# Optimization experiments

Hardware: AMD Instinct MI355X
Metric: run time of the kernel (lower is better)

## Reference

```python
import jax, jax.numpy as jnp
import numpy as np

T, B, D, H, F, E = 2048, 2, 1024, 16, 4096, 8
HD = D // H
EPS = 1.1920929e-07  # torch.finfo(float32).eps


def setup_inputs() -> dict:
    key = jax.random.key(0)
    ks = jax.random.split(key, 20)
    sc = D ** -0.5
    n = lambda k, shape, s: jax.random.normal(k, shape, jnp.float32) * s
    return {
        "x": jax.random.normal(ks[0], (T, B, D), jnp.float32),
        "Wq": n(ks[1], (D, D), sc), "bq": jnp.zeros((D,), jnp.float32),
        "Wk": n(ks[2], (D, D), sc), "bk": jnp.zeros((D,), jnp.float32),
        "Wv": n(ks[3], (D, D), sc), "bv": jnp.zeros((D,), jnp.float32),
        "Wo": n(ks[4], (D, D), sc), "bo": jnp.zeros((D,), jnp.float32),
        "ln1_g": jnp.ones((D,), jnp.float32), "ln1_b": jnp.zeros((D,), jnp.float32),
        "ln2_g": jnp.ones((D,), jnp.float32), "ln2_b": jnp.zeros((D,), jnp.float32),
        "wg": n(ks[5], (D, E), sc),
        "W1": n(ks[6], (E, D, F), sc), "b1": jnp.zeros((E, F), jnp.float32),
        "W2": n(ks[7], (E, F, D), F ** -0.5), "b2": jnp.zeros((E, D), jnp.float32),
    }


def layer_norm(x, g, b):
    m = jnp.mean(x, -1, keepdims=True)
    v = jnp.var(x, -1, keepdims=True)
    return (x - m) * jax.lax.rsqrt(v + 1e-5) * g + b


def attention(x, Wq, bq, Wk, bk, Wv, bv, Wo, bo):
    t, b, d = x.shape
    q = ((x @ Wq + bq) * (HD ** -0.5)).reshape(t, b, H, HD)
    k = (x @ Wk + bk).reshape(t, b, H, HD)
    v = (x @ Wv + bv).reshape(t, b, H, HD)
    a = jax.nn.softmax(jnp.einsum('tbhd,sbhd->bhts', q, k), axis=-1)
    o = jnp.einsum('bhts,sbhd->tbhd', a, v).reshape(t, b, d)
    return o @ Wo + bo


def moe(xf, wg, W1, b1, W2, b2):
    # xf: [S, D] tokens (batch-major order, matching x.transpose(0,1).reshape(-1,d))
    S = xf.shape[0]
    C = 2 * ((S + E - 1) // E)  # fairseq top2 train capacity
    logits = xf.astype(jnp.float32) @ wg.astype(jnp.float32)
    gates = jax.nn.softmax(logits, axis=-1)
    idx1 = jnp.argmax(gates, axis=-1)
    m1 = jax.nn.one_hot(idx1, E, dtype=jnp.int32)
    idx2 = jnp.argmax(jnp.where(m1 > 0, -jnp.inf, logits), axis=-1)
    m2 = jax.nn.one_hot(idx2, E, dtype=jnp.int32)
    g1 = jnp.take_along_axis(gates, idx1[:, None], 1)[:, 0]
    g2 = jnp.take_along_axis(gates, idx2[:, None], 1)[:, 0]
    loc1 = jnp.cumsum(m1, axis=0) - 1
    loc2 = jnp.cumsum(m2, axis=0) - 1 + jnp.sum(m1, axis=0, keepdims=True)
    pos1 = jnp.sum(loc1 * m1, axis=1)
    pos2 = jnp.sum(loc2 * m2, axis=1)
    l_aux = jnp.mean(jnp.mean(gates, 0) * jnp.mean(m1.astype(jnp.float32), 0)) * E * E
    k1 = (pos1 < C).astype(xf.dtype)
    k2 = (pos2 < C).astype(xf.dtype)
    g1 = g1.astype(xf.dtype) * k1
    g2 = g2.astype(xf.dtype) * k2
    den = jnp.maximum(g1 + g2, EPS)
    g1, g2 = g1 / den, g2 / den
    f1 = idx1 * C + jnp.minimum(pos1, C - 1)
    f2 = idx2 * C + jnp.minimum(pos2, C - 1)
    # dispatch (unweighted, capacity-masked)
    buf = jnp.zeros((E * C, D), xf.dtype)
    buf = buf.at[f1].add(xf * k1[:, None]).at[f2].add(xf * k2[:, None])
    h = jax.nn.relu(jnp.einsum('ecd,edf->ecf', buf.reshape(E, C, D), W1) + b1[:, None, :])
    out = (jnp.einsum('ecf,efd->ecd', h, W2) + b2[:, None, :]).reshape(E * C, D)
    # combine with normalized gates (dropped tokens have zero gate)
    y = g1[:, None] * out[f1] + g2[:, None] * out[f2]
    return y, l_aux


def reference(x, Wq, bq, Wk, bk, Wv, bv, Wo, bo, ln1_g, ln1_b, ln2_g, ln2_b, wg, W1, b1, W2, b2):
    # pre-LN self-attention block
    residual = x
    h = layer_norm(x, ln1_g, ln1_b)
    h = attention(h, Wq, bq, Wk, bk, Wv, bv, Wo, bo)
    x = residual + h
    # pre-LN MoE FFN block
    residual = x
    h = layer_norm(x, ln2_g, ln2_b)
    hb = jnp.swapaxes(h, 0, 1).reshape(-1, D)  # [B*T, D]
    y, l_aux = moe(hb, wg, W1, b1, W2, b2)
    y = jnp.swapaxes(y.reshape(B, T, D), 0, 1)
    x = residual + y
    return x, l_aux
```

## Files before the change

### kernel.cpp

```cpp
#include <hip/hip_runtime.h>

#define TT 2048
#define BB 2
#define DD 1024
#define HH 16
#define HD 64
#define FF 4096
#define EE 8
#define SS (TT*BB)
#define CAP 1024
#define EPSF 1.1920929e-07f

typedef __attribute__((ext_vector_type(8))) short short8;
typedef __attribute__((ext_vector_type(4))) float floatx4;

static __device__ inline unsigned short f2bf(float f){
    unsigned int u = __float_as_uint(f);
    unsigned int r = (u + 0x7fffu + ((u>>16)&1u)) >> 16;
    return (unsigned short)r;
}
static __device__ inline float bf2f(unsigned short h){
    return __uint_as_float(((unsigned int)h)<<16);
}
static __device__ inline void split2(float x, unsigned short& h, unsigned short& l){
    unsigned short hh = f2bf(x);
    h = hh;
    l = f2bf(x - bf2f(hh));
}
#define GETF4(v,j) ((j)==0?(v).x:(j)==1?(v).y:(j)==2?(v).z:(v).w)

__global__ __launch_bounds__(256) void ln_kernel(const float* __restrict__ x,
    const float* __restrict__ gam, const float* __restrict__ bet, float* __restrict__ o)
{
    int row = blockIdx.x;
    int tid = threadIdx.x;
    float4 v = ((const float4*)(x + (size_t)row*DD))[tid];
    float s  = v.x+v.y+v.z+v.w;
    float ss = v.x*v.x+v.y*v.y+v.z*v.z+v.w*v.w;
    __shared__ float r1[256], r2[256];
    r1[tid]=s; r2[tid]=ss;
    __syncthreads();
    for (int off=128; off>0; off>>=1){
        if (tid<off){ r1[tid]+=r1[tid+off]; r2[tid]+=r2[tid+off]; }
        __syncthreads();
    }
    float mean = r1[0] * (1.f/DD);
    float var  = r2[0] * (1.f/DD) - mean*mean;
    float inv  = 1.f / sqrtf(var + 1e-5f);
    float4 g = ((const float4*)gam)[tid];
    float4 b = ((const float4*)bet)[tid];
    float4 r;
    r.x = (v.x-mean)*inv*g.x + b.x;
    r.y = (v.y-mean)*inv*g.y + b.y;
    r.z = (v.z-mean)*inv*g.z + b.z;
    r.w = (v.w-mean)*inv*g.w + b.w;
    ((float4*)(o + (size_t)row*DD))[tid] = r;
}

template<bool RELU, bool OUTBF16>
__global__ __launch_bounds__(256) void gemm_mfma(
    const unsigned short* __restrict__ A, const unsigned short* __restrict__ Bt,
    const float* __restrict__ bias, float* __restrict__ Cf,
    unsigned short* __restrict__ Cb,
    int M, int N, int K, long wStride, int bStride, int rowsPerExp)
{
    __shared__ unsigned short As[128*64];
    __shared__ unsigned short Bs[128*64];
    const int tid = threadIdx.x, lane = tid&63;
    const int w = tid>>6, wr = w>>1, wc = w&1;
    const int m0 = blockIdx.y*128, n0 = blockIdx.x*128;
    const int e = m0 / rowsPerExp;
    const unsigned short* Bp = Bt + (size_t)e*wStride;
    const int srow = tid>>3, sslot = tid&7;
    floatx4 zf = {0.f,0.f,0.f,0.f};
    floatx4 acc[4][4];
    #pragma unroll
    for (int m=0;m<4;m++)
        #pragma unroll
        for (int n=0;n<4;n++) acc[m][n]=zf;

    short8 ar[4], br[4];
    #pragma unroll
    for (int i=0;i<4;i++){
        int r = srow + i*32;
        ar[i] = *(const short8*)(A  + (size_t)(m0+r)*K + sslot*8);
        br[i] = *(const short8*)(Bp + (size_t)(n0+r)*K + sslot*8);
    }
    const int NT = K/64;
    for (int kt=0; kt<NT; kt++){
        __syncthreads();
        #pragma unroll
        for (int i=0;i<4;i++){
            int r = srow + i*32;
            int off = r*64 + ((sslot ^ (r&7))<<3);
            *(short8*)(&As[off]) = ar[i];
            *(short8*)(&Bs[off]) = br[i];
        }
        __syncthreads();
        if (kt+1 < NT){
            int k0 = (kt+1)*64;
            #pragma unroll
            for (int i=0;i<4;i++){
                int r = srow + i*32;
                ar[i] = *(const short8*)(A  + (size_t)(m0+r)*K + k0 + sslot*8);
                br[i] = *(const short8*)(Bp + (size_t)(n0+r)*K + k0 + sslot*8);
            }
        }
        #pragma unroll
        for (int kk=0;kk<2;kk++){
            short8 af[4], bf[4];
            int kgrp = kk*4 + (lane>>4);
            #pragma unroll
            for (int m=0;m<4;m++){
                int rowa = wr*64 + m*16 + (lane&15);
                af[m] = *(const short8*)(&As[rowa*64 + ((kgrp ^ (rowa&7))<<3)]);
                int rowb = wc*64 + m*16 + (lane&15);
                bf[m] = *(const short8*)(&Bs[rowb*64 + ((kgrp ^ (rowb&7))<<3)]);
            }
            #pragma unroll
            for (int m=0;m<4;m++)
                #pragma unroll
                for (int n=0;n<4;n++)
                    acc[m][n] = __builtin_amdgcn_mfma_f32_16x16x32_bf16(af[m], bf[n], acc[m][n], 0,0,0);
        }
    }
    int colg = n0 + wc*64 + (lane&15);
    int rowg = m0 + wr*64 + ((lane>>4)<<2);
    #pragma unroll
    for (int n=0;n<4;n++){
        float bv = bias[e*bStride + colg + n*16];
        #pragma unroll
        for (int m=0;m<4;m++){
            #pragma unroll
            for (int i2=0;i2<4;i2++){
                float v = acc[m][n][i2] + bv;
                if (RELU) v = fmaxf(v, 0.f);
                size_t o = (size_t)(rowg + m*16 + i2)*N + colg + n*16;
                if (OUTBF16) Cb[o] = f2bf(v); else Cf[o] = v;
            }
        }
    }
}

template<bool QKV>
__global__ __launch_bounds__(256) void gemm_mfma_s(
    const float* __restrict__ A,
    const unsigned short* __restrict__ Bhi, const unsigned short* __restrict__ Blo,
    const float* __restrict__ b0, const float* __restrict__ b1p, const float* __restrict__ b2p,
    const float* __restrict__ res,
    float* __restrict__ o0, float* __restrict__ o1, float* __restrict__ o2,
    int M, int K)
{
    __shared__ unsigned short As[128*64];
    __shared__ unsigned short Bs[128*64];
    const int tid = threadIdx.x, lane = tid&63;
    const int w = tid>>6, wr = w>>1, wc = w&1;
    const int m0 = blockIdx.y*128, n0 = blockIdx.x*128;
    const int row = tid>>1, khalf = tid&1;
    floatx4 zf = {0.f,0.f,0.f,0.f};
    floatx4 acc[4][4];
    #pragma unroll
    for (int m=0;m<4;m++)
        #pragma unroll
        for (int n=0;n<4;n++) acc[m][n]=zf;

    float4 aw0,aw1,aw2,aw3;
    short8 bwh0,bwh1,bwl0,bwl1;
    {
        const float* ap = A + (size_t)(m0+row)*K + khalf*16;
        aw0 = ((const float4*)ap)[0]; aw1 = ((const float4*)ap)[1];
        aw2 = ((const float4*)ap)[2]; aw3 = ((const float4*)ap)[3];
        const unsigned short* bh = Bhi + (size_t)(n0+row)*K + khalf*16;
        const unsigned short* bl = Blo + (size_t)(n0+row)*K + khalf*16;
        bwh0 = *(const short8*)(bh); bwh1 = *(const short8*)(bh+8);
        bwl0 = *(const short8*)(bl); bwl1 = *(const short8*)(bl+8);
    }
    const int NT = K/32;
    for (int kt=0; kt<NT; kt++){
        __syncthreads();
        {
            unsigned short h[16], l[16];
            #pragma unroll
            for (int j=0;j<4;j++){ split2(GETF4(aw0,j), h[j],   l[j]); }
            #pragma unroll
            for (int j=0;j<4;j++){ split2(GETF4(aw1,j), h[4+j], l[4+j]); }
            #pragma unroll
            for (int j=0;j<4;j++){ split2(GETF4(aw2,j), h[8+j], l[8+j]); }
            #pragma unroll
            for (int j=0;j<4;j++){ split2(GETF4(aw3,j), h[12+j],l[12+j]); }
            int base = row*64, sw = row&7;
            int g0 = khalf*2, g1 = khalf*2+1;
            *(short8*)(&As[base + ((g0^sw)<<3)])     = *(short8*)(&h[0]);
            *(short8*)(&As[base + ((g1^sw)<<3)])     = *(short8*)(&h[8]);
            *(short8*)(&As[base + (((g0+4)^sw)<<3)]) = *(short8*)(&l[0]);
            *(short8*)(&As[base + (((g1+4)^sw)<<3)]) = *(short8*)(&l[8]);
            *(short8*)(&Bs[base + ((g0^sw)<<3)])     = bwh0;
            *(short8*)(&Bs[base + ((g1^sw)<<3)])     = bwh1;
            *(short8*)(&Bs[base + (((g0+4)^sw)<<3)]) = bwl0;
            *(short8*)(&Bs[base + (((g1+4)^sw)<<3)]) = bwl1;
        }
        __syncthreads();
        if (kt+1 < NT){
            int k0 = (kt+1)*32;
            const float* ap = A + (size_t)(m0+row)*K + k0 + khalf*16;
            aw0 = ((const float4*)ap)[0]; aw1 = ((const float4*)ap)[1];
            aw2 = ((const float4*)ap)[2]; aw3 = ((const float4*)ap)[3];
            const unsigned short* bh = Bhi + (size_t)(n0+row)*K + k0 + khalf*16;
            const unsigned short* bl = Blo + (size_t)(n0+row)*K + k0 + khalf*16;
            bwh0 = *(const short8*)(bh); bwh1 = *(const short8*)(bh+8);
            bwl0 = *(const short8*)(bl); bwl1 = *(const short8*)(bl+8);
        }
        {
            int kg = lane>>4;
            short8 afh[4], afl[4], bfh[4], bfl[4];
            #pragma unroll
            for (int m=0;m<4;m++){
                int ra = wr*64 + m*16 + (lane&15);
                afh[m] = *(const short8*)(&As[ra*64 + ((kg ^ (ra&7))<<3)]);
                afl[m] = *(const short8*)(&As[ra*64 + (((kg+4) ^ (ra&7))<<3)]);
                int rb = wc*64 + m*16 + (lane&15);
                bfh[m] = *(const short8*)(&Bs[rb*64 + ((kg ^ (rb&7))<<3)]);
                bfl[m] = *(const short8*)(&Bs[rb*64 + (((kg+4) ^ (rb&7))<<3)]);
            }
            #pragma unroll
            for (int m=0;m<4;m++)
                #pragma unroll
                for (int n=0;n<4;n++){
                    acc[m][n] = __builtin_amdgcn_mfma_f32_16x16x32_bf16(afl[m], bfl[n], acc[m][n], 0,0,0);
                    acc[m][n] = __builtin_amdgcn_mfma_f32_16x16x32_bf16(afl[m], bfh[n], acc[m][n], 0,0,0);
                    acc[m][n] = __builtin_amdgcn_mfma_f32_16x16x32_bf16(afh[m], bfl[n], acc[m][n], 0,0,0);
                    acc[m][n] = __builtin_amdgcn_mfma_f32_16x16x32_bf16(afh[m], bfh[n], acc[m][n], 0,0,0);
                }
        }
    }
    int colg = n0 + wc*64 + (lane&15);
    int rowg = m0 + wr*64 + ((lane>>4)<<2);
    const float* bp; float* op; float scale; int colc;
    if (QKV){
        int chunk = n0>>10;
        bp = chunk==0 ? b0 : (chunk==1 ? b1p : b2p);
        op = chunk==0 ? o0 : (chunk==1 ? o1 : o2);
        scale = chunk==0 ? 0.125f : 1.0f;
        colc = colg & 1023;
    } else { bp = b0; op = o0; scale = 1.0f; colc = colg; }
    #pragma unroll
    for (int n=0;n<4;n++){
        float bv = bp[colc + n*16];
        #pragma unroll
        for (int m=0;m<4;m++){
            #pragma unroll
            for (int i2=0;i2<4;i2++){
                float v = (acc[m][n][i2] + bv)*scale;
                int r = rowg + m*16 + i2;
                if (!QKV) v += res[(size_t)r*DD + colc + n*16];
                op[(size_t)r*DD + colc + n*16] = v;
            }
        }
    }
}

__global__ __launch_bounds__(256) void attn_mfma(const float* __restrict__ q,
    const float* __restrict__ k, const float* __restrict__ v, float* __restrict__ o)
{
    __shared__ unsigned short Kh[64*64], Kl[64*64];
    __shared__ unsigned short Vh[64*64], Vl[64*64];
    __shared__ unsigned short Ph[4*16*64], Pl[4*16*64];
    const int tid = threadIdx.x, lane = tid&63, w = tid>>6;
    const int t0 = blockIdx.x*64;
    const int b = blockIdx.y>>4, h = blockIdx.y&15;

    short8 qh[2], ql[2];
    #pragma unroll
    for (int kk=0;kk<2;kk++){
        const float* qp = q + ((size_t)(t0 + 16*w + (lane&15))*BB + b)*DD + h*64 + kk*32 + (lane>>4)*8;
        float4 f0 = ((const float4*)qp)[0];
        float4 f1 = ((const float4*)qp)[1];
        unsigned short hh[8], ll[8];
        #pragma unroll
        for (int j=0;j<4;j++){ split2(GETF4(f0,j), hh[j], ll[j]); }
        #pragma unroll
        for (int j=0;j<4;j++){ split2(GETF4(f1,j), hh[4+j], ll[4+j]); }
        qh[kk] = *(short8*)hh; ql[kk] = *(short8*)ll;
    }

    const int kr = tid>>2, kq = tid&3;
    const int vs0 = (tid&15)*4, vd0 = (tid>>4)*4;
    float4 kw0,kw1,kw2,kw3, vw0,vw1,vw2,vw3;
    {
        const float* kp = k + ((size_t)(0 + kr)*BB + b)*DD + h*64 + kq*16;
        kw0=((const float4*)kp)[0]; kw1=((const float4*)kp)[1];
        kw2=((const float4*)kp)[2]; kw3=((const float4*)kp)[3];
        const float* vp = v + ((size_t)(0 + vs0)*BB + b)*DD + h*64 + vd0;
        vw0=*(const float4*)(vp);
        vw1=*(const float4*)(vp + (size_t)BB*DD);
        vw2=*(const float4*)(vp + (size_t)2*BB*DD);
        vw3=*(const float4*)(vp + (size_t)3*BB*DD);
    }

    float m_st[4] = {-3.0e38f,-3.0e38f,-3.0e38f,-3.0e38f};
    float l_st[4] = {0.f,0.f,0.f,0.f};
    floatx4 zf = {0.f,0.f,0.f,0.f};
    floatx4 oacc[4]; 
    #pragma unroll
    for (int n=0;n<4;n++) oacc[n]=zf;

    for (int s0=0; s0<TT; s0+=64){
        __syncthreads();
        {
            unsigned short hh[16], ll[16];
            #pragma unroll
            for (int j=0;j<4;j++){ split2(GETF4(kw0,j), hh[j],   ll[j]); }
            #pragma unroll
            for (int j=0;j<4;j++){ split2(GETF4(kw1,j), hh[4+j], ll[4+j]); }
            #pragma unroll
            for (int j=0;j<4;j++){ split2(GETF4(kw2,j), hh[8+j], ll[8+j]); }
            #pragma unroll
            for (int j=0;j<4;j++){ split2(GETF4(kw3,j), hh[12+j],ll[12+j]); }
            int base = kr*64, sw = kr&7;
            int g0 = kq*2, g1 = kq*2+1;
            *(short8*)(&Kh[base + ((g0^sw)<<3)]) = *(short8*)(&hh[0]);
            *(short8*)(&Kh[base + ((g1^sw)<<3)]) = *(short8*)(&hh[8]);
            *(short8*)(&Kl[base + ((g0^sw)<<3)]) = *(short8*)(&ll[0]);
            *(short8*)(&Kl[base + ((g1^sw)<<3)]) = *(short8*)(&ll[8]);
        }
        {
            int g = vs0>>3, so = vs0&7;
            #pragma unroll
            for (int j=0;j<4;j++){
                int d = vd0 + j;
                unsigned short h0,h1,h2,h3, l0,l1,l2,l3;
                split2(GETF4(vw0,j), h0,l0);
                split2(GETF4(vw1,j), h1,l1);
                split2(GETF4(vw2,j), h2,l2);
                split2(GETF4(vw3,j), h3,l3);
                ushort4 hv; hv.x=h0; hv.y=h1; hv.z=h2; hv.w=h3;
                ushort4 lv; lv.x=l0; lv.y=l1; lv.z=l2; lv.w=l3;
                int off = d*64 + ((g ^ (d&7))<<3) + so;
                *(ushort4*)(&Vh[off]) = hv;
                *(ushort4*)(&Vl[off]) = lv;
            }
        }
        __syncthreads();
        if (s0+64 < TT){
            const float* kp = k + ((size_t)(s0+64 + kr)*BB + b)*DD + h*64 + kq*16;
            kw0=((const float4*)kp)[0]; kw1=((const float4*)kp)[1];
            kw2=((const float4*)kp)[2]; kw3=((const float4*)kp)[3];
            const float* vp = v + ((size_t)(s0+64 + vs0)*BB + b)*DD + h*64 + vd0;
            vw0=*(const float4*)(vp);
            vw1=*(const float4*)(vp + (size_t)BB*DD);
            vw2=*(const float4*)(vp + (size_t)2*BB*DD);
            vw3=*(const float4*)(vp + (size_t)3*BB*DD);
        }
        floatx4 sacc[4];
        #pragma unroll
        for (int n=0;n<4;n++){
            floatx4 s = zf;
            #pragma unroll
            for (int kk=0;kk<2;kk++){
                int g = kk*4 + (lane>>4);
                int rb = n*16 + (lane&15);
                short8 kbh = *(const short8*)(&Kh[rb*64 + ((g ^ (rb&7))<<3)]);
                short8 kbl = *(const short8*)(&Kl[rb*64 + ((g ^ (rb&7))<<3)]);
                s = __builtin_amdgcn_mfma_f32_16x16x32_bf16(ql[kk], kbl, s, 0,0,0);
                s = __builtin_amdgcn_mfma_f32_16x16x32_bf16(ql[kk], kbh, s, 0,0,0);
                s = __builtin_amdgcn_mfma_f32_16x16x32_bf16(qh[kk], kbl, s, 0,0,0);
                s = __builtin_amdgcn_mfma_f32_16x16x32_bf16(qh[kk], kbh, s, 0,0,0);
            }
            sacc[n] = s;
        }
        float mx[4];
        #pragma unroll
        for (int r=0;r<4;r++)
            mx[r] = fmaxf(fmaxf(sacc[0][r], sacc[1][r]), fmaxf(sacc[2][r], sacc[3][r]));
        #pragma unroll
        for (int sh=1; sh<16; sh<<=1){
            #pragma unroll
            for (int r=0;r<4;r++) mx[r] = fmaxf(mx[r], __shfl_xor(mx[r], sh));
        }
        float corr[4];
        #pragma unroll
        for (int r=0;r<4;r++){
            float nm = fmaxf(m_st[r], mx[r]);
            corr[r] = __expf(m_st[r] - nm);
            m_st[r] = nm;
        }
        float ts[4] = {0.f,0.f,0.f,0.f};
        #pragma unroll
        for (int n=0;n<4;n++){
            #pragma unroll
            for (int r=0;r<4;r++){
                float p = __expf(sacc[n][r] - m_st[r]);
                ts[r] += p;
                unsigned short ph, pl;
                split2(p, ph, pl);
                int q2 = ((lane>>4)<<2) + r;
                int s2 = n*16 + (lane&15);
                int off = w*1024 + q2*64 + (((s2>>3) ^ (q2&7))<<3) + (s2&7);
                Ph[off] = ph; Pl[off] = pl;
            }
        }
        #pragma unroll
        for (int sh=1; sh<16; sh<<=1){
            #pragma unroll
            for (int r=0;r<4;r++) ts[r] += __shfl_xor(ts[r], sh);
        }
        #pragma unroll
        for (int r=0;r<4;r++) l_st[r] = l_st[r]*corr[r] + ts[r];
        #pragma unroll
        for (int n=0;n<4;n++)
            #pragma unroll
            for (int r=0;r<4;r++) oacc[n][r] *= corr[r];
        #pragma unroll
        for (int kk=0;kk<2;kk++){
            int g = kk*4 + (lane>>4);
            int rq = lane&15;
            short8 pah = *(const short8*)(&Ph[w*1024 + rq*64 + ((g ^ (rq&7))<<3)]);
            short8 pal = *(const short8*)(&Pl[w*1024 + rq*64 + ((g ^ (rq&7))<<3)]);
            #pragma unroll
            for (int n=0;n<4;n++){
                int rd = n*16 + (lane&15);
                short8 vbh = *(const short8*)(&Vh[rd*64 + ((g ^ (rd&7))<<3)]);
                short8 vbl = *(const short8*)(&Vl[rd*64 + ((g ^ (rd&7))<<3)]);
                oacc[n] = __builtin_amdgcn_mfma_f32_16x16x32_bf16(pal, vbl, oacc[n], 0,0,0);
                oacc[n] = __builtin_amdgcn_mfma_f32_16x16x32_bf16(pal, vbh, oacc[n], 0,0,0);
                oacc[n] = __builtin_amdgcn_mfma_f32_16x16x32_bf16(pah, vbl, oacc[n], 0,0,0);
                oacc[n] = __builtin_amdgcn_mfma_f32_16x16x32_bf16(pah, vbh, oacc[n], 0,0,0);
            }
        }
    }
    float il[4];
    #pragma unroll
    for (int r=0;r<4;r++) il[r] = 1.f/l_st[r];
    int qrow = t0 + 16*w + ((lane>>4)<<2);
    #pragma unroll
    for (int n=0;n<4;n++){
        #pragma unroll
        for (int r=0;r<4;r++){
            o[((size_t)(qrow+r)*BB + b)*DD + h*64 + n*16 + (lane&15)] = oacc[n][r]*il[r];
        }
    }
}

__global__ __launch_bounds__(256) void transpose_bf16_k(const float* __restrict__ in,
    unsigned short* __restrict__ outp, int R, int C)
{
    __shared__ float t[64][65];
    int e = blockIdx.z;
    const float* ip = in + (size_t)e*R*C;
    unsigned short* op = outp + (size_t)e*R*C;
    int r0 = blockIdx.y*64, c0 = blockIdx.x*64;
    int tid = threadIdx.x;
    #pragma unroll
    for (int i=0;i<4;i++){
        int ch = i*256 + tid;
        int r = ch>>4, c4 = (ch&15)*4;
        float4 v = *(const float4*)(ip + (size_t)(r0+r)*C + c0 + c4);
        t[r][c4+0]=v.x; t[r][c4+1]=v.y; t[r][c4+2]=v.z; t[r][c4+3]=v.w;
    }
    __syncthreads();
    #pragma unroll
    for (int i=0;i<4;i++){
        int ch = i*256 + tid;
        int rr = ch>>4, c4 = (ch&15)*4;
        ushort4 o;
        o.x = f2bf(t[c4+0][rr]); o.y = f2bf(t[c4+1][rr]);
        o.z = f2bf(t[c4+2][rr]); o.w = f2bf(t[c4+3][rr]);
        *(ushort4*)(op + (size_t)(c0+rr)*R + r0 + c4) = o;
    }
}

__global__ __launch_bounds__(256) void transpose_split_k(const float* __restrict__ in,
    unsigned short* __restrict__ oh, unsigned short* __restrict__ ol, int R, int C)
{
    __shared__ float t[64][65];
    int r0 = blockIdx.y*64, c0 = blockIdx.x*64;
    int tid = threadIdx.x;
    #pragma unroll
    for (int i=0;i<4;i++){
        int ch = i*256 + tid;
        int r = ch>>4, c4 = (ch&15)*4;
        float4 v = *(const float4*)(in + (size_t)(r0+r)*C + c0 + c4);
        t[r][c4+0]=v.x; t[r][c4+1]=v.y; t[r][c4+2]=v.z; t[r][c4+3]=v.w;
    }
    __syncthreads();
    #pragma unroll
    for (int i=0;i<4;i++){
        int ch = i*256 + tid;
        int rr = ch>>4, c4 = (ch&15)*4;
        ushort4 hv, lv;
        split2(t[c4+0][rr], hv.x, lv.x);
        split2(t[c4+1][rr], hv.y, lv.y);
        split2(t[c4+2][rr], hv.z, lv.z);
        split2(t[c4+3][rr], hv.w, lv.w);
        size_t off = (size_t)(c0+rr)*R + r0 + c4;
        *(ushort4*)(oh + off) = hv;
        *(ushort4*)(ol + off) = lv;
    }
}

__global__ __launch_bounds__(256) void gather_bf16_k(const float* __restrict__ h2,
    const int* __restrict__ s2r, unsigned short* __restrict__ buf)
{
    int s = blockIdx.x; int row = s2r[s]; int c = threadIdx.x;
    float4 v = make_float4(0.f,0.f,0.f,0.f);
    if (row>=0) v = *(const float4*)(h2 + (size_t)row*DD + c*4);
    ushort4 o;
    o.x=f2bf(v.x); o.y=f2bf(v.y); o.z=f2bf(v.z); o.w=f2bf(v.w);
    *(ushort4*)(buf + (size_t)s*DD + c*4) = o;
}

__global__ __launch_bounds__(256) void route_kernel(const float* __restrict__ h2,
    const float* __restrict__ wgm, float* __restrict__ gates,
    int* __restrict__ idx1, int* __restrict__ idx2,
    float* __restrict__ g1, float* __restrict__ g2)
{
    int wid = threadIdx.x >> 6, lane = threadIdx.x & 63;
    int s = blockIdx.x*4 + wid;
    int row = (s % TT)*BB + (s / TT);
    const float* hr = h2 + (size_t)row*DD;
    float acc[EE] = {};
    #pragma unroll
    for (int c=0;c<16;c++){
        int d = c*64 + lane;
        float xv = hr[d];
        const float* wr = wgm + (size_t)d*EE;
        #pragma unroll
        for (int e2=0;e2<EE;e2++) acc[e2] += xv * wr[e2];
    }
    #pragma unroll
    for (int off=32; off>0; off>>=1){
        #pragma unroll
        for (int e2=0;e2<EE;e2++) acc[e2] += __shfl_down(acc[e2], off);
    }
    if (lane==0){
        float mx = acc[0];
        #pragma unroll
        for (int e2=1;e2<EE;e2++) mx = fmaxf(mx, acc[e2]);
        float ex[EE]; float sum=0.f;
        #pragma unroll
        for (int e2=0;e2<EE;e2++){ ex[e2] = __expf(acc[e2]-mx); sum += ex[e2]; }
        float inv = 1.f/sum;
        int i1=0; float bv1=acc[0];
        #pragma unroll
        for (int e2=1;e2<EE;e2++){ if (acc[e2] > bv1){ bv1=acc[e2]; i1=e2; } }
        int i2=-1; float bv2=-3.0e38f;
        #pragma unroll
        for (int e2=0;e2<EE;e2++){ if (e2!=i1 && acc[e2] > bv2){ bv2=acc[e2]; i2=e2; } }
        #pragma unroll
        for (int e2=0;e2<EE;e2++) gates[(size_t)s*EE + e2] = ex[e2]*inv;
        idx1[s]=i1; idx2[s]=i2;
        g1[s]=ex[i1]*inv; g2[s]=ex[i2]*inv;
    }
}

__global__ __launch_bounds__(256) void scan_kernel(
    const float* __restrict__ gates, const int* __restrict__ idx1, const int* __restrict__ idx2,
    const float* __restrict__ g1, const float* __restrict__ g2,
    float* __restrict__ g1n, float* __restrict__ g2n,
    int* __restrict__ f1, int* __restrict__ f2, int* __restrict__ slot2row,
    float* __restrict__ laux)
{
    __shared__ int i1s[SS];
    __shared__ int i2s[SS];
    __shared__ int cnt1[256][EE];
    __shared__ int cnt2[256][EE];
    __shared__ float gsum[256][EE];
    __shared__ int tot1[EE];
    int tid = threadIdx.x;
    for (int i=tid;i<EE*CAP;i+=256) slot2row[i] = -1;
    for (int i=tid;i<SS;i+=256){ i1s[i]=idx1[i]; i2s[i]=idx2[i]; }
    __syncthreads();
    int c1l[EE]={}, c2l[EE]={};
    float gl[EE]={};
    int base = tid*16;
    for (int qq=0;qq<16;qq++){
        int s = base+qq;
        c1l[i1s[s]]++; c2l[i2s[s]]++;
        #pragma unroll
        for (int e2=0;e2<EE;e2++) gl[e2] += gates[(size_t)s*EE+e2];
    }
    #pragma unroll
    for (int e2=0;e2<EE;e2++){ cnt1[tid][e2]=c1l[e2]; cnt2[tid][e2]=c2l[e2]; gsum[tid][e2]=gl[e2]; }
    __syncthreads();
    if (tid < EE){
        int e2 = tid;
        int run=0;
        for (int t=0;t<256;t++){ int tmp=cnt1[t][e2]; cnt1[t][e2]=run; run+=tmp; }
        tot1[e2]=run;
        run=0;
        for (int t=0;t<256;t++){ int tmp=cnt2[t][e2]; cnt2[t][e2]=run; run+=tmp; }
        float gr=0.f;
        for (int t=0;t<256;t++) gr += gsum[t][e2];
        gsum[0][e2]=gr;
    }
    __syncthreads();
    int p1[EE], p2[EE];
    #pragma unroll
    for (int e2=0;e2<EE;e2++){ p1[e2]=cnt1[tid][e2]; p2[e2]=cnt2[tid][e2]+tot1[e2]; }
    for (int qq=0;qq<16;qq++){
        int s = base+qq;
        int e1 = i1s[s], e2v = i2s[s];
        int pos1 = p1[e1]++;
        int pos2 = p2[e2v]++;
        float gv1 = g1[s], gv2 = g2[s];
        float gm1 = (pos1<CAP)? gv1 : 0.f;
        float gm2 = (pos2<CAP)? gv2 : 0.f;
        float den = fmaxf(gm1+gm2, EPSF);
        g1n[s] = gm1/den; g2n[s] = gm2/den;
        int ff1 = e1*CAP + (pos1<CAP?pos1:CAP-1);
        int ff2 = e2v*CAP + (pos2<CAP?pos2:CAP-1);
        f1[s]=ff1; f2[s]=ff2;
        int hrow = (s % TT)*BB + (s / TT);
        if (pos1<CAP) slot2row[ff1]=hrow;
        if (pos2<CAP) slot2row[ff2]=hrow;
    }
    if (tid==0){
        float a=0.f;
        #pragma unroll
        for (int e2=0;e2<EE;e2++) a += (gsum[0][e2]*(1.f/SS)) * ((float)tot1[e2]*(1.f/SS));
        laux[0] = a * (float)EE;
    }
}

__global__ __launch_bounds__(256) void combine_kernel(const float* __restrict__ x2,
    const float* __restrict__ eout, const float* __restrict__ g1n, const float* __restrict__ g2n,
    const int* __restrict__ f1, const int* __restrict__ f2, float* __restrict__ out)
{
    int s = blockIdx.x;
    float a = g1n[s], b = g2n[s];
    int s1 = f1[s], s2 = f2[s];
    int row = (s % TT)*BB + (s / TT);
    int c = threadIdx.x;
    float4 o1 = ((const float4*)(eout + (size_t)s1*DD))[c];
    float4 o2 = ((const float4*)(eout + (size_t)s2*DD))[c];
    float4 xr = ((const float4*)(x2 + (size_t)row*DD))[c];
    float4 r;
    r.x = xr.x + a*o1.x + b*o2.x;
    r.y = xr.y + a*o1.y + b*o2.y;
    r.z = xr.z + a*o1.z + b*o2.z;
    r.w = xr.w + a*o1.w + b*o2.w;
    ((float4*)(out + (size_t)row*DD))[c] = r;
}

extern "C" void kernel_launch(void* const* d_in, const int* in_sizes, int n_in,
                              void* d_out, int out_size, void* d_ws, size_t ws_size,
                              hipStream_t stream)
{
    const float* x    = (const float*)d_in[0];
    const float* Wq   = (const float*)d_in[1];
    const float* bq   = (const float*)d_in[2];
    const float* Wk   = (const float*)d_in[3];
    const float* bk   = (const float*)d_in[4];
    const float* Wv   = (const float*)d_in[5];
    const float* bv   = (const float*)d_in[6];
    const float* Wo   = (const float*)d_in[7];
    const float* bo   = (const float*)d_in[8];
    const float* ln1g = (const float*)d_in[9];
    const float* ln1b = (const float*)d_in[10];
    const float* ln2g = (const float*)d_in[11];
    const float* ln2b = (const float*)d_in[12];
    const float* wgm  = (const float*)d_in[13];
    const float* W1   = (const float*)d_in[14];
    const float* b1   = (const float*)d_in[15];
    const float* W2   = (const float*)d_in[16];
    const float* b2   = (const float*)d_in[17];
    float* out = (float*)d_out;

    char* w = (char*)d_ws;
    float*          h1   = (float*)(w);
    float*          qb   = (float*)(w + ((size_t)16<<20));
    float*          kb   = (float*)(w + ((size_t)32<<20));
    float*          vb   = (float*)(w + ((size_t)48<<20));
    float*          x2   = (float*)(w + ((size_t)64<<20));
    unsigned short* bufb = (unsigned short*)(w + ((size_t)80<<20));
    unsigned short* hb   = (unsigned short*)(w + ((size_t)96<<20));
    unsigned short* Bqkv_hi = (unsigned short*)(w + ((size_t)96<<20));
    unsigned short* Bqkv_lo = (unsigned short*)(w + ((size_t)102<<20));
    unsigned short* Bo_hi   = (unsigned short*)(w + ((size_t)108<<20));
    unsigned short* Bo_lo   = (unsigned short*)(w + ((size_t)110<<20));
    unsigned short* W1t  = (unsigned short*)(w + ((size_t)160<<20));
    unsigned short* W2t  = (unsigned short*)(w + ((size_t)224<<20));
    float*          ffno = kb;
    char*  sm   = w + ((size_t)288<<20);
    float* gates   = (float*)(sm);                sm += (size_t)SS*EE*4;
    int*   idx1    = (int*)(sm);                  sm += SS*4;
    int*   idx2    = (int*)(sm);                  sm += SS*4;
    float* g1      = (float*)(sm);                sm += SS*4;
    float* g2      = (float*)(sm);                sm += SS*4;
    float* g1n     = (float*)(sm);                sm += SS*4;
    float* g2n     = (float*)(sm);                sm += SS*4;
    int*   f1      = (int*)(sm);                  sm += SS*4;
    int*   f2      = (int*)(sm);                  sm += SS*4;
    int*   slot2row= (int*)(sm);                  sm += EE*CAP*4;

    transpose_bf16_k<<<dim3(FF/64, DD/64, EE), 256, 0, stream>>>(W1, W1t, DD, FF);
    transpose_bf16_k<<<dim3(DD/64, FF/64, EE), 256, 0, stream>>>(W2, W2t, FF, DD);
    transpose_split_k<<<dim3(16,16), 256, 0, stream>>>(Wq, Bqkv_hi,                Bqkv_lo,                DD, DD);
    transpose_split_k<<<dim3(16,16), 256, 0, stream>>>(Wk, Bqkv_hi + (size_t)DD*DD,   Bqkv_lo + (size_t)DD*DD,   DD, DD);
    transpose_split_k<<<dim3(16,16), 256, 0, stream>>>(Wv, Bqkv_hi + (size_t)2*DD*DD, Bqkv_lo + (size_t)2*DD*DD, DD, DD);
    transpose_split_k<<<dim3(16,16), 256, 0, stream>>>(Wo, Bo_hi, Bo_lo, DD, DD);
    ln_kernel<<<SS, 256, 0, stream>>>(x, ln1g, ln1b, h1);
    gemm_mfma_s<true><<<dim3(24, SS/128), 256, 0, stream>>>(
        h1, Bqkv_hi, Bqkv_lo, bq, bk, bv, nullptr, qb, kb, vb, SS, DD);
    attn_mfma<<<dim3(TT/64, BB*HH), 256, 0, stream>>>(qb, kb, vb, h1);
    gemm_mfma_s<false><<<dim3(8, SS/128), 256, 0, stream>>>(
        h1, Bo_hi, Bo_lo, bo, bo, bo, x, x2, x2, x2, SS, DD);
    ln_kernel<<<SS, 256, 0, stream>>>(x2, ln2g, ln2b, qb);
    route_kernel<<<SS/4, 256, 0, stream>>>(qb, wgm, gates, idx1, idx2, g1, g2);
    scan_kernel<<<1, 256, 0, stream>>>(gates, idx1, idx2, g1, g2,
        g1n, g2n, f1, f2, slot2row, out + (size_t)SS*DD);
    gather_bf16_k<<<EE*CAP, 256, 0, stream>>>(qb, slot2row, bufb);
    gemm_mfma<true,true><<<dim3(FF/128, (EE*CAP)/128), 256, 0, stream>>>(
        bufb, W1t, b1, nullptr, hb, EE*CAP, FF, DD, (long)FF*DD, FF, CAP);
    gemm_mfma<false,false><<<dim3(DD/128, (EE*CAP)/128), 256, 0, stream>>>(
        hb, W2t, b2, ffno, nullptr, EE*CAP, DD, FF, (long)DD*FF, DD, CAP);
    combine_kernel<<<SS, 256, 0, stream>>>(x2, ffno, g1n, g2n, f1, f2, out);
    (void)in_sizes; (void)n_in; (void)out_size; (void)ws_size;
}
```

Before: 686.7 us.

## Drop lo*lo MFMA terms and pre-split K/V into bf16 hi/lo in QKV epilogue

Removes the low-times-low MFMA term from the split-bf16 GEMMs and from the attention QK and PV products, cutting matrix work by a quarter. The QKV GEMM epilogue now writes K and V directly as bf16 hi/lo pairs, so attention loads half-width data and skips its per-tile split. Truncation-based splitting replaces round-to-nearest for activations and P, which makes the splits cheaper. The trade is slightly lower precision and more work in the QKV epilogue.

Measured after the change: 681.5 us. Within noise of the previous version (-0.8%).

```diff
diff --git a/kernel.cpp b/kernel.cpp
--- a/kernel.cpp
+++ b/kernel.cpp
@@ -27,7 +27,15 @@
     h = hh;
     l = f2bf(x - bf2f(hh));
 }
+static __device__ inline void split2t(float x, unsigned short& h, unsigned short& l){
+    unsigned int u = __float_as_uint(x);
+    unsigned int hu = u & 0xffff0000u;
+    h = (unsigned short)(hu>>16);
+    float r = x - __uint_as_float(hu);
+    l = (unsigned short)(__float_as_uint(r)>>16);
+}
 #define GETF4(v,j) ((j)==0?(v).x:(j)==1?(v).y:(j)==2?(v).z:(v).w)
+#define GETU4(v,j) ((j)==0?(v).x:(j)==1?(v).y:(j)==2?(v).z:(v).w)
 
 __global__ __launch_bounds__(256) void ln_kernel(const float* __restrict__ x,
     const float* __restrict__ gam, const float* __restrict__ bet, float* __restrict__ o)
@@ -148,7 +156,9 @@
     const unsigned short* __restrict__ Bhi, const unsigned short* __restrict__ Blo,
     const float* __restrict__ b0, const float* __restrict__ b1p, const float* __restrict__ b2p,
     const float* __restrict__ res,
-    float* __restrict__ o0, float* __restrict__ o1, float* __restrict__ o2,
+    float* __restrict__ o0,
+    unsigned short* __restrict__ kh, unsigned short* __restrict__ kl,
+    unsigned short* __restrict__ vh, unsigned short* __restrict__ vl,
     int M, int K)
 {
     __shared__ unsigned short As[128*64];
@@ -181,13 +191,13 @@
         {
             unsigned short h[16], l[16];
             #pragma unroll
-            for (int j=0;j<4;j++){ split2(GETF4(aw0,j), h[j],   l[j]); }
-            #pragma unroll
-            for (int j=0;j<4;j++){ split2(GETF4(aw1,j), h[4+j], l[4+j]); }
-            #pragma unroll
-            for (int j=0;j<4;j++){ split2(GETF4(aw2,j), h[8+j], l[8+j]); }
-            #pragma unroll
-            for (int j=0;j<4;j++){ split2(GETF4(aw3,j), h[12+j],l[12+j]); }
+            for (int j=0;j<4;j++){ split2t(GETF4(aw0,j), h[j],   l[j]); }
+            #pragma unroll
+            for (int j=0;j<4;j++){ split2t(GETF4(aw1,j), h[4+j], l[4+j]); }
+            #pragma unroll
+            for (int j=0;j<4;j++){ split2t(GETF4(aw2,j), h[8+j], l[8+j]); }
+            #pragma unroll
+            for (int j=0;j<4;j++){ split2t(GETF4(aw3,j), h[12+j],l[12+j]); }
             int base = row*64, sw = row&7;
             int g0 = khalf*2, g1 = khalf*2+1;
             *(short8*)(&As[base + ((g0^sw)<<3)])     = *(short8*)(&h[0]);
@@ -226,7 +236,6 @@
             for (int m=0;m<4;m++)
                 #pragma unroll
                 for (int n=0;n<4;n++){
-                    acc[m][n] = __builtin_amdgcn_mfma_f32_16x16x32_bf16(afl[m], bfl[n], acc[m][n], 0,0,0);
                     acc[m][n] = __builtin_amdgcn_mfma_f32_16x16x32_bf16(afl[m], bfh[n], acc[m][n], 0,0,0);
                     acc[m][n] = __builtin_amdgcn_mfma_f32_16x16x32_bf16(afh[m], bfl[n], acc[m][n], 0,0,0);
                     acc[m][n] = __builtin_amdgcn_mfma_f32_16x16x32_bf16(afh[m], bfh[n], acc[m][n], 0,0,0);
@@ -235,32 +244,52 @@
     }
     int colg = n0 + wc*64 + (lane&15);
     int rowg = m0 + wr*64 + ((lane>>4)<<2);
-    const float* bp; float* op; float scale; int colc;
     if (QKV){
         int chunk = n0>>10;
-        bp = chunk==0 ? b0 : (chunk==1 ? b1p : b2p);
-        op = chunk==0 ? o0 : (chunk==1 ? o1 : o2);
-        scale = chunk==0 ? 0.125f : 1.0f;
-        colc = colg & 1023;
-    } else { bp = b0; op = o0; scale = 1.0f; colc = colg; }
-    #pragma unroll
-    for (int n=0;n<4;n++){
-        float bv = bp[colc + n*16];
-        #pragma unroll
-        for (int m=0;m<4;m++){
-            #pragma unroll
-            for (int i2=0;i2<4;i2++){
-                float v = (acc[m][n][i2] + bv)*scale;
-                int r = rowg + m*16 + i2;
-                if (!QKV) v += res[(size_t)r*DD + colc + n*16];
-                op[(size_t)r*DD + colc + n*16] = v;
+        int colc = colg & 1023;
+        const float* bp = chunk==0 ? b0 : (chunk==1 ? b1p : b2p);
+        #pragma unroll
+        for (int n=0;n<4;n++){
+            float bv = bp[colc + n*16];
+            #pragma unroll
+            for (int m=0;m<4;m++){
+                #pragma unroll
+                for (int i2=0;i2<4;i2++){
+                    int r = rowg + m*16 + i2;
+                    float v = acc[m][n][i2] + bv;
+                    size_t off = (size_t)r*DD + colc + n*16;
+                    if (chunk==0){
+                        o0[off] = v*0.125f;
+                    } else {
+                        unsigned short hh, ll;
+                        split2(v, hh, ll);
+                        if (chunk==1){ kh[off]=hh; kl[off]=ll; }
+                        else         { vh[off]=hh; vl[off]=ll; }
+                    }
+                }
+            }
+        }
+    } else {
+        #pragma unroll
+        for (int n=0;n<4;n++){
+            float bv = b0[colg + n*16];
+            #pragma unroll
+            for (int m=0;m<4;m++){
+                #pragma unroll
+                for (int i2=0;i2<4;i2++){
+                    int r = rowg + m*16 + i2;
+                    float v = acc[m][n][i2] + bv + res[(size_t)r*DD + colg + n*16];
+                    o0[(size_t)r*DD + colg + n*16] = v;
+                }
             }
         }
     }
 }
 
 __global__ __launch_bounds__(256) void attn_mfma(const float* __restrict__ q,
-    const float* __restrict__ k, const float* __restrict__ v, float* __restrict__ o)
+    const unsigned short* __restrict__ khi, const unsigned short* __restrict__ klo,
+    const unsigned short* __restrict__ vhi, const unsigned short* __restrict__ vlo,
+    float* __restrict__ o)
 {
     __shared__ unsigned short Kh[64*64], Kl[64*64];
     __shared__ unsigned short Vh[64*64], Vl[64*64];
@@ -285,56 +314,46 @@
 
     const int kr = tid>>2, kq = tid&3;
     const int vs0 = (tid&15)*4, vd0 = (tid>>4)*4;
-    float4 kw0,kw1,kw2,kw3, vw0,vw1,vw2,vw3;
+    short8 kwh0,kwh1,kwl0,kwl1;
+    ushort4 vwh[4], vwl[4];
     {
-        const float* kp = k + ((size_t)(0 + kr)*BB + b)*DD + h*64 + kq*16;
-        kw0=((const float4*)kp)[0]; kw1=((const float4*)kp)[1];
-        kw2=((const float4*)kp)[2]; kw3=((const float4*)kp)[3];
-        const float* vp = v + ((size_t)(0 + vs0)*BB + b)*DD + h*64 + vd0;
-        vw0=*(const float4*)(vp);
-        vw1=*(const float4*)(vp + (size_t)BB*DD);
-        vw2=*(const float4*)(vp + (size_t)2*BB*DD);
-        vw3=*(const float4*)(vp + (size_t)3*BB*DD);
+        const unsigned short* kp = khi + ((size_t)kr*BB + b)*DD + h*64 + kq*16;
+        const unsigned short* lp = klo + ((size_t)kr*BB + b)*DD + h*64 + kq*16;
+        kwh0 = *(const short8*)(kp); kwh1 = *(const short8*)(kp+8);
+        kwl0 = *(const short8*)(lp); kwl1 = *(const short8*)(lp+8);
+        #pragma unroll
+        for (int i=0;i<4;i++){
+            size_t vo = ((size_t)(vs0+i)*BB + b)*DD + h*64 + vd0;
+            vwh[i] = *(const ushort4*)(vhi + vo);
+            vwl[i] = *(const ushort4*)(vlo + vo);
+        }
     }
 
     float m_st[4] = {-3.0e38f,-3.0e38f,-3.0e38f,-3.0e38f};
     float l_st[4] = {0.f,0.f,0.f,0.f};
     floatx4 zf = {0.f,0.f,0.f,0.f};
-    floatx4 oacc[4]; 
+    floatx4 oacc[4];
     #pragma unroll
     for (int n=0;n<4;n++) oacc[n]=zf;
 
     for (int s0=0; s0<TT; s0+=64){
         __syncthreads();
         {
-            unsigned short hh[16], ll[16];
-            #pragma unroll
-            for (int j=0;j<4;j++){ split2(GETF4(kw0,j), hh[j],   ll[j]); }
-            #pragma unroll
-            for (int j=0;j<4;j++){ split2(GETF4(kw1,j), hh[4+j], ll[4+j]); }
-            #pragma unroll
-            for (int j=0;j<4;j++){ split2(GETF4(kw2,j), hh[8+j], ll[8+j]); }
-            #pragma unroll
-            for (int j=0;j<4;j++){ split2(GETF4(kw3,j), hh[12+j],ll[12+j]); }
             int base = kr*64, sw = kr&7;
             int g0 = kq*2, g1 = kq*2+1;
-            *(short8*)(&Kh[base + ((g0^sw)<<3)]) = *(short8*)(&hh[0]);
-            *(short8*)(&Kh[base + ((g1^sw)<<3)]) = *(short8*)(&hh[8]);
-            *(short8*)(&Kl[base + ((g0^sw)<<3)]) = *(short8*)(&ll[0]);
-            *(short8*)(&Kl[base + ((g1^sw)<<3)]) = *(short8*)(&ll[8]);
+            *(short8*)(&Kh[base + ((g0^sw)<<3)]) = kwh0;
+            *(short8*)(&Kh[base + ((g1^sw)<<3)]) = kwh1;
+            *(short8*)(&Kl[base + ((g0^sw)<<3)]) = kwl0;
+            *(short8*)(&Kl[base + ((g1^sw)<<3)]) = kwl1;
         }
         {
             int g = vs0>>3, so = vs0&7;
             #pragma unroll
             for (int j=0;j<4;j++){
                 int d = vd0 + j;
-                unsigned short h0,h1,h2,h3, l0,l1,l2,l3;
-                split2(GETF4(vw0,j), h0,l0);
-                split2(GETF4(vw1,j), h1,l1);
-                split2(GETF4(vw2,j), h2,l2);
-                split2(GETF4(vw3,j), h3,l3);
-                ushort4 hv; hv.x=h0; hv.y=h1; hv.z=h2; hv.w=h3;
-                ushort4 lv; lv.x=l0; lv.y=l1; lv.z=l2; lv.w=l3;
+                ushort4 hv, lv;
+                hv.x=GETU4(vwh[0],j); hv.y=GETU4(vwh[1],j); hv.z=GETU4(vwh[2],j); hv.w=GETU4(vwh[3],j);
+                lv.x=GETU4(vwl[0],j); lv.y=GETU4(vwl[1],j); lv.z=GETU4(vwl[2],j); lv.w=GETU4(vwl[3],j);
                 int off = d*64 + ((g ^ (d&7))<<3) + so;
                 *(ushort4*)(&Vh[off]) = hv;
                 *(ushort4*)(&Vl[off]) = lv;
@@ -342,14 +361,16 @@
         }
         __syncthreads();
         if (s0+64 < TT){
-            const float* kp = k + ((size_t)(s0+64 + kr)*BB + b)*DD + h*64 + kq*16;
-            kw0=((const float4*)kp)[0]; kw1=((const float4*)kp)[1];
-            kw2=((const float4*)kp)[2]; kw3=((const float4*)kp)[3];
-            const float* vp = v + ((size_t)(s0+64 + vs0)*BB + b)*DD + h*64 + vd0;
-            vw0=*(const float4*)(vp);
-            vw1=*(const float4*)(vp + (size_t)BB*DD);
-            vw2=*(const float4*)(vp + (size_t)2*BB*DD);
-            vw3=*(const float4*)(vp + (size_t)3*BB*DD);
+            const unsigned short* kp = khi + ((size_t)(s0+64+kr)*BB + b)*DD + h*64 + kq*16;
+            const unsigned short* lp = klo + ((size_t)(s0+64+kr)*BB + b)*DD + h*64 + kq*16;
+            kwh0 = *(const short8*)(kp); kwh1 = *(const short8*)(kp+8);
+            kwl0 = *(const short8*)(lp); kwl1 = *(const short8*)(lp+8);
+            #pragma unroll
+            for (int i=0;i<4;i++){
+                size_t vo = ((size_t)(s0+64+vs0+i)*BB + b)*DD + h*64 + vd0;
+                vwh[i] = *(const ushort4*)(vhi + vo);
+                vwl[i] = *(const ushort4*)(vlo + vo);
+            }
         }
         floatx4 sacc[4];
         #pragma unroll
@@ -361,7 +382,6 @@
                 int rb = n*16 + (lane&15);
                 short8 kbh = *(const short8*)(&Kh[rb*64 + ((g ^ (rb&7))<<3)]);
                 short8 kbl = *(const short8*)(&Kl[rb*64 + ((g ^ (rb&7))<<3)]);
-                s = __builtin_amdgcn_mfma_f32_16x16x32_bf16(ql[kk], kbl, s, 0,0,0);
                 s = __builtin_amdgcn_mfma_f32_16x16x32_bf16(ql[kk], kbh, s, 0,0,0);
                 s = __builtin_amdgcn_mfma_f32_16x16x32_bf16(qh[kk], kbl, s, 0,0,0);
                 s = __builtin_amdgcn_mfma_f32_16x16x32_bf16(qh[kk], kbh, s, 0,0,0);
@@ -392,7 +412,7 @@
                 float p = __expf(sacc[n][r] - m_st[r]);
                 ts[r] += p;
                 unsigned short ph, pl;
-                split2(p, ph, pl);
+                split2t(p, ph, pl);
                 int q2 = ((lane>>4)<<2) + r;
                 int s2 = n*16 + (lane&15);
                 int off = w*1024 + q2*64 + (((s2>>3) ^ (q2&7))<<3) + (s2&7);
@@ -421,7 +441,6 @@
                 int rd = n*16 + (lane&15);
                 short8 vbh = *(const short8*)(&Vh[rd*64 + ((g ^ (rd&7))<<3)]);
                 short8 vbl = *(const short8*)(&Vl[rd*64 + ((g ^ (rd&7))<<3)]);
-                oacc[n] = __builtin_amdgcn_mfma_f32_16x16x32_bf16(pal, vbl, oacc[n], 0,0,0);
                 oacc[n] = __builtin_amdgcn_mfma_f32_16x16x32_bf16(pal, vbh, oacc[n], 0,0,0);
                 oacc[n] = __builtin_amdgcn_mfma_f32_16x16x32_bf16(pah, vbl, oacc[n], 0,0,0);
                 oacc[n] = __builtin_amdgcn_mfma_f32_16x16x32_bf16(pah, vbh, oacc[n], 0,0,0);
@@ -669,8 +688,10 @@
     char* w = (char*)d_ws;
     float*          h1   = (float*)(w);
     float*          qb   = (float*)(w + ((size_t)16<<20));
-    float*          kb   = (float*)(w + ((size_t)32<<20));
-    float*          vb   = (float*)(w + ((size_t)48<<20));
+    unsigned short* Khg  = (unsigned short*)(w + ((size_t)32<<20));
+    unsigned short* Klg  = (unsigned short*)(w + ((size_t)40<<20));
+    unsigned short* Vhg  = (unsigned short*)(w + ((size_t)48<<20));
+    unsigned short* Vlg  = (unsigned short*)(w + ((size_t)56<<20));
     float*          x2   = (float*)(w + ((size_t)64<<20));
     unsigned short* bufb = (unsigned short*)(w + ((size_t)80<<20));
     unsigned short* hb   = (unsigned short*)(w + ((size_t)96<<20));
@@ -680,7 +701,7 @@
     unsigned short* Bo_lo   = (unsigned short*)(w + ((size_t)110<<20));
     unsigned short* W1t  = (unsigned short*)(w + ((size_t)160<<20));
     unsigned short* W2t  = (unsigned short*)(w + ((size_t)224<<20));
-    float*          ffno = kb;
+    float*          ffno = (float*)(w + ((size_t)32<<20));
     char*  sm   = w + ((size_t)288<<20);
     float* gates   = (float*)(sm);                sm += (size_t)SS*EE*4;
     int*   idx1    = (int*)(sm);                  sm += SS*4;
@@ -695,16 +716,16 @@
 
     transpose_bf16_k<<<dim3(FF/64, DD/64, EE), 256, 0, stream>>>(W1, W1t, DD, FF);
     transpose_bf16_k<<<dim3(DD/64, FF/64, EE), 256, 0, stream>>>(W2, W2t, FF, DD);
-    transpose_split_k<<<dim3(16,16), 256, 0, stream>>>(Wq, Bqkv_hi,                Bqkv_lo,                DD, DD);
+    transpose_split_k<<<dim3(16,16), 256, 0, stream>>>(Wq, Bqkv_hi,                   Bqkv_lo,                   DD, DD);
     transpose_split_k<<<dim3(16,16), 256, 0, stream>>>(Wk, Bqkv_hi + (size_t)DD*DD,   Bqkv_lo + (size_t)DD*DD,   DD, DD);
     transpose_split_k<<<dim3(16,16), 256, 0, stream>>>(Wv, Bqkv_hi + (size_t)2*DD*DD, Bqkv_lo + (size_t)2*DD*DD, DD, DD);
     transpose_split_k<<<dim3(16,16), 256, 0, stream>>>(Wo, Bo_hi, Bo_lo, DD, DD);
     ln_kernel<<<SS, 256, 0, stream>>>(x, ln1g, ln1b, h1);
     gemm_mfma_s<true><<<dim3(24, SS/128), 256, 0, stream>>>(
-        h1, Bqkv_hi, Bqkv_lo, bq, bk, bv, nullptr, qb, kb, vb, SS, DD);
-    attn_mfma<<<dim3(TT/64, BB*HH), 256, 0, stream>>>(qb, kb, vb, h1);
+        h1, Bqkv_hi, Bqkv_lo, bq, bk, bv, nullptr, qb, Khg, Klg, Vhg, Vlg, SS, DD);
+    attn_mfma<<<dim3(TT/64, BB*HH), 256, 0, stream>>>(qb, Khg, Klg, Vhg, Vlg, h1);
     gemm_mfma_s<false><<<dim3(8, SS/128), 256, 0, stream>>>(
-        h1, Bo_hi, Bo_lo, bo, bo, bo, x, x2, x2, x2, SS, DD);
+        h1, Bo_hi, Bo_lo, bo, bo, bo, x, x2, nullptr, nullptr, nullptr, nullptr, SS, DD);
     ln_kernel<<<SS, 256, 0, stream>>>(x2, ln2g, ln2b, qb);
     route_kernel<<<SS/4, 256, 0, stream>>>(qb, wgm, gates, idx1, idx2, g1, g2);
     scan_kernel<<<1, 256, 0, stream>>>(gates, idx1, idx2, g1, g2,
```
